# Performance work log

Measured on AMD Instinct MI355X. Metric: run time of the kernel, lower is better.

## Reference

```python
import jax, jax.numpy as jnp
import numpy as np

B, M, V, TOPK = 64, 8192, 128, 64
EPS = 1e-8  # stands in for LOG_EPS and F.cosine_similarity eps clamp


def setup_inputs() -> dict:
    key = jax.random.key(0)
    k1, k2 = jax.random.split(key)
    stdev = 1.0 / np.sqrt(M + V)
    memory = jax.random.uniform(k1, (B, M, V), dtype=jnp.float32, minval=-stdev, maxval=stdev)
    v = jax.random.normal(k2, (B, V), dtype=jnp.float32)
    return {"memory": memory, "v": v, "topk": TOPK}


def reference(memory, v, topk):
    # --- similarity(v, topk): cosine similarity of query against each memory slot ---
    a = memory + EPS                      # (B, M, V)
    b = v + EPS                           # (B, V)
    num = jnp.einsum('bmv,bv->bm', a, b)  # (B, M)
    denom = jnp.maximum(
        jnp.linalg.norm(a, axis=-1) * jnp.linalg.norm(b, axis=-1)[:, None], EPS
    )
    sim = num / denom                     # (B, M), unnormalized addressing weights
    # topk masking: torch zeroes the (M - topk) smallest entries via scatter_;
    # equivalently keep values >= the topk-th largest value (ties negligible for floats)
    kth = jax.lax.top_k(sim, topk)[0][:, -1:]   # (B, 1)
    w = jnp.where(sim >= kth, sim, jnp.zeros((), sim.dtype))
    # --- write(w, v): rank-1 outer-product update ---
    new_mem = memory + w[:, :, None] * v[:, None, :]   # (B, M, V)
    # --- read(w): weighted sum over slots; torch returns (B,1,1,V) via double unsqueeze ---
    read = jnp.einsum('bm,bmv->bv', w, new_mem)[:, None, None, :]
    return read
```

## Files before the change

kernel.cpp:

```cpp
#include <hip/hip_runtime.h>
#include <hip/hip_bf16.h>

#define B_DIM 64
#define M_DIM 8192
#define V_DIM 128
#define EPS 1e-8f
#define KCAP 2048

__device__ __forceinline__ unsigned int f2key(float f) {
    unsigned int u = __float_as_uint(f);
    return (u & 0x80000000u) ? ~u : (u | 0x80000000u);
}
__device__ __forceinline__ float key2f(unsigned int k) {
    return (k & 0x80000000u) ? __uint_as_float(k & 0x7FFFFFFFu)
                             : __uint_as_float(~k);
}

__global__ void sim_kernel(const float* __restrict__ mem,
                           const float* __restrict__ v,
                           unsigned int* __restrict__ keys_out) {
    const int b    = blockIdx.y;
    const int m0   = blockIdx.x * 64;
    const int tid  = threadIdx.x;
    const int wave = tid >> 6;
    const int lane = tid & 63;
    const int rw   = lane >> 4;
    const int sub  = lane & 15;

    __shared__ float vs[V_DIM];
    __shared__ float s_invbn;

    if (tid < V_DIM) vs[tid] = v[b * V_DIM + tid] + EPS;
    __syncthreads();

    if (tid < 64) {
        float x0 = vs[tid], x1 = vs[tid + 64];
        float s = x0 * x0 + x1 * x1;
#pragma unroll
        for (int mk = 32; mk; mk >>= 1) s += __shfl_xor(s, mk, 64);
        if (tid == 0) s_invbn = 1.0f / sqrtf(s);
    }
    __syncthreads();

    const float4 va = *reinterpret_cast<const float4*>(&vs[sub * 4]);
    const float4 vb = *reinterpret_cast<const float4*>(&vs[sub * 4 + 64]);
    const float invbn = s_invbn;

#pragma unroll
    for (int t = 0; t < 4; ++t) {
        const int m = m0 + t * 16 + wave * 4 + rw;
        const float4* rp =
            reinterpret_cast<const float4*>(mem + ((size_t)b * M_DIM + m) * V_DIM);
        float4 x0 = rp[sub];
        float4 x1 = rp[sub + 16];
        float a0 = x0.x + EPS, a1 = x0.y + EPS, a2 = x0.z + EPS, a3 = x0.w + EPS;
        float a4 = x1.x + EPS, a5 = x1.y + EPS, a6 = x1.z + EPS, a7 = x1.w + EPS;
        float dot = a0 * va.x + a1 * va.y + a2 * va.z + a3 * va.w
                  + a4 * vb.x + a5 * vb.y + a6 * vb.z + a7 * vb.w;
        float ss  = a0 * a0 + a1 * a1 + a2 * a2 + a3 * a3
                  + a4 * a4 + a5 * a5 + a6 * a6 + a7 * a7;
#pragma unroll
        for (int mk = 8; mk; mk >>= 1) {
            dot += __shfl_xor(dot, mk, 16);
            ss  += __shfl_xor(ss,  mk, 16);
        }
        if (sub == 0) {
            float sim = dot * rsqrtf(ss) * invbn;
            keys_out[(size_t)b * M_DIM + m] = f2key(sim);
        }
    }
}

__global__ void topk_read_kernel(const float* __restrict__ mem,
                                 const float* __restrict__ v,
                                 const unsigned int* __restrict__ keys_in,
                                 const int* __restrict__ topk_p,
                                 float* __restrict__ out) {
    const int b   = blockIdx.x;
    const int tid = threadIdx.x;
    const int NT  = 256;
    const int wv  = tid >> 6;

    __shared__ unsigned int keys[M_DIM];
    __shared__ unsigned int hist[4 * 256];
    __shared__ int          sfx[256];
    __shared__ unsigned int s_prefix;
    __shared__ int s_k;
    __shared__ int s_cnt;
    __shared__ int   s_idx[KCAP];
    __shared__ float s_w[KCAP];
    __shared__ float s_sumw2;
    __shared__ float s_acc[256];

    for (int i = tid; i < M_DIM; i += NT)
        keys[i] = keys_in[(size_t)b * M_DIM + i];
    if (tid == 0) { s_prefix = 0u; s_k = topk_p[0]; s_cnt = 0; }
    __syncthreads();

    for (int p = 3; p >= 0; --p) {
#pragma unroll
        for (int h = tid; h < 1024; h += NT) hist[h] = 0u;
        __syncthreads();
        const unsigned int dm = (p == 3) ? 0u : (0xFFFFFFFFu << ((p + 1) * 8));
        const unsigned int pf = s_prefix;
        const int k_cur = s_k;
        for (int i = tid; i < M_DIM; i += NT) {
            unsigned int ky = keys[i];
            if ((ky & dm) == pf)
                atomicAdd(&hist[wv * 256 + ((ky >> (p * 8)) & 0xFFu)], 1u);
        }
        __syncthreads();
        int c = (int)(hist[tid] + hist[256 + tid] + hist[512 + tid] + hist[768 + tid]);
        sfx[tid] = c;
        __syncthreads();
#pragma unroll
        for (int off = 1; off < 256; off <<= 1) {
            int x = (tid + off < 256) ? sfx[tid + off] : 0;
            __syncthreads();
            sfx[tid] += x;
            __syncthreads();
        }
        int S_t  = sfx[tid];
        int S_t1 = (tid < 255) ? sfx[tid + 1] : 0;
        if (S_t >= k_cur && S_t1 < k_cur) {
            s_prefix = pf | ((unsigned int)tid << (p * 8));
            s_k = k_cur - S_t1;
        }
        __syncthreads();
    }
    const unsigned int kth = s_prefix;

    for (int i = tid; i < M_DIM; i += NT) {
        unsigned int ky = keys[i];
        if (ky >= kth) {
            int pos = atomicAdd(&s_cnt, 1);
            if (pos < KCAP) { s_idx[pos] = i; s_w[pos] = key2f(ky); }
        }
    }
    __syncthreads();
    const int cnt = min(s_cnt, KCAP);

    if (tid < 64) {
        float s = 0.f;
        for (int i = tid; i < cnt; i += 64) s += s_w[i] * s_w[i];
#pragma unroll
        for (int mk = 32; mk; mk >>= 1) s += __shfl_xor(s, mk, 64);
        if (tid == 0) s_sumw2 = s;
    }
    __syncthreads();

    const int col  = tid & 127;
    const int half = tid >> 7;
    const float* mb = mem + (size_t)b * M_DIM * V_DIM;
    float a0 = 0.f, a1 = 0.f, a2 = 0.f, a3 = 0.f;
    int j = half;
    for (; j + 6 < cnt; j += 8) {
        a0 += s_w[j]     * mb[(size_t)s_idx[j]     * V_DIM + col];
        a1 += s_w[j + 2] * mb[(size_t)s_idx[j + 2] * V_DIM + col];
        a2 += s_w[j + 4] * mb[(size_t)s_idx[j + 4] * V_DIM + col];
        a3 += s_w[j + 6] * mb[(size_t)s_idx[j + 6] * V_DIM + col];
    }
    for (; j < cnt; j += 2)
        a0 += s_w[j] * mb[(size_t)s_idx[j] * V_DIM + col];
    s_acc[tid] = (a0 + a1) + (a2 + a3);
    __syncthreads();
    if (tid < 128)
        out[b * V_DIM + tid] =
            s_acc[tid] + s_acc[tid + 128] + s_sumw2 * v[b * V_DIM + tid];
}

extern "C" void kernel_launch(void* const* d_in, const int* in_sizes, int n_in,
                              void* d_out, int out_size, void* d_ws, size_t ws_size,
                              hipStream_t stream) {
    const float* mem  = (const float*)d_in[0];
    const float* v    = (const float*)d_in[1];
    const int*   topk = (const int*)d_in[2];
    float* out        = (float*)d_out;
    unsigned int* keys = (unsigned int*)d_ws;

    dim3 grid1(M_DIM / 64, B_DIM);
    sim_kernel<<<grid1, 256, 0, stream>>>(mem, v, keys);

    topk_read_kernel<<<B_DIM, 256, 0, stream>>>(mem, v, keys, topk, out);
}
```

Baseline: 378.7 us.

## Widen top-k block, aggregate histogram atomics, and coarsen similarity blocks

The similarity kernel now handles 256 rows per block instead of 64, and it no longer adds EPS to each memory element, which removes some arithmetic but slightly changes the numerics of the cosine. The top-k/read kernel moves from 256 to 1024 threads per block and loads keys with vector loads. Histogram updates are aggregated per wave with ballot instead of being spread over per-wave histograms, and the suffix-scan over 256 buckets is replaced by one wave using shuffles. These changes target the latency-bound selection kernel, which runs only 64 blocks, and cut barrier-heavy scans, at the cost of more complex ballot loops and a small numerical deviation.

Measured after the change: 387.3 us. 2.3% more time.

```diff
diff --git a/kernel.cpp b/kernel.cpp
--- a/kernel.cpp
+++ b/kernel.cpp
@@ -6,6 +6,7 @@
 #define V_DIM 128
 #define EPS 1e-8f
 #define KCAP 2048
+#define NT2 1024
 
 __device__ __forceinline__ unsigned int f2key(float f) {
     unsigned int u = __float_as_uint(f);
@@ -20,7 +21,7 @@
                            const float* __restrict__ v,
                            unsigned int* __restrict__ keys_out) {
     const int b    = blockIdx.y;
-    const int m0   = blockIdx.x * 64;
+    const int m0   = blockIdx.x * 256;
     const int tid  = threadIdx.x;
     const int wave = tid >> 6;
     const int lane = tid & 63;
@@ -46,19 +47,17 @@
     const float4 vb = *reinterpret_cast<const float4*>(&vs[sub * 4 + 64]);
     const float invbn = s_invbn;
 
-#pragma unroll
-    for (int t = 0; t < 4; ++t) {
+#pragma unroll 4
+    for (int t = 0; t < 16; ++t) {
         const int m = m0 + t * 16 + wave * 4 + rw;
         const float4* rp =
             reinterpret_cast<const float4*>(mem + ((size_t)b * M_DIM + m) * V_DIM);
         float4 x0 = rp[sub];
         float4 x1 = rp[sub + 16];
-        float a0 = x0.x + EPS, a1 = x0.y + EPS, a2 = x0.z + EPS, a3 = x0.w + EPS;
-        float a4 = x1.x + EPS, a5 = x1.y + EPS, a6 = x1.z + EPS, a7 = x1.w + EPS;
-        float dot = a0 * va.x + a1 * va.y + a2 * va.z + a3 * va.w
-                  + a4 * vb.x + a5 * vb.y + a6 * vb.z + a7 * vb.w;
-        float ss  = a0 * a0 + a1 * a1 + a2 * a2 + a3 * a3
-                  + a4 * a4 + a5 * a5 + a6 * a6 + a7 * a7;
+        float dot = x0.x * va.x + x0.y * va.y + x0.z * va.z + x0.w * va.w
+                  + x1.x * vb.x + x1.y * vb.y + x1.z * vb.z + x1.w * vb.w;
+        float ss  = x0.x * x0.x + x0.y * x0.y + x0.z * x0.z + x0.w * x0.w
+                  + x1.x * x1.x + x1.y * x1.y + x1.z * x1.z + x1.w * x1.w;
 #pragma unroll
         for (int mk = 8; mk; mk >>= 1) {
             dot += __shfl_xor(dot, mk, 16);
@@ -71,66 +70,88 @@
     }
 }
 
-__global__ void topk_read_kernel(const float* __restrict__ mem,
-                                 const float* __restrict__ v,
-                                 const unsigned int* __restrict__ keys_in,
-                                 const int* __restrict__ topk_p,
-                                 float* __restrict__ out) {
-    const int b   = blockIdx.x;
-    const int tid = threadIdx.x;
-    const int NT  = 256;
-    const int wv  = tid >> 6;
+__global__ __launch_bounds__(NT2)
+void topk_read_kernel(const float* __restrict__ mem,
+                      const float* __restrict__ v,
+                      const unsigned int* __restrict__ keys_in,
+                      const int* __restrict__ topk_p,
+                      float* __restrict__ out) {
+    const int b    = blockIdx.x;
+    const int tid  = threadIdx.x;
+    const int lane = tid & 63;
+    const int wv   = tid >> 6;
 
     __shared__ unsigned int keys[M_DIM];
-    __shared__ unsigned int hist[4 * 256];
-    __shared__ int          sfx[256];
+    __shared__ unsigned int hist[256];
     __shared__ unsigned int s_prefix;
     __shared__ int s_k;
     __shared__ int s_cnt;
     __shared__ int   s_idx[KCAP];
     __shared__ float s_w[KCAP];
     __shared__ float s_sumw2;
-    __shared__ float s_acc[256];
-
-    for (int i = tid; i < M_DIM; i += NT)
-        keys[i] = keys_in[(size_t)b * M_DIM + i];
+    __shared__ float s_acc[NT2];
+
+    {
+        const uint4* kin = reinterpret_cast<const uint4*>(keys_in + (size_t)b * M_DIM);
+        uint4* kl = reinterpret_cast<uint4*>(keys);
+        for (int i = tid; i < M_DIM / 4; i += NT2) kl[i] = kin[i];
+    }
     if (tid == 0) { s_prefix = 0u; s_k = topk_p[0]; s_cnt = 0; }
     __syncthreads();
 
     for (int p = 3; p >= 0; --p) {
-#pragma unroll
-        for (int h = tid; h < 1024; h += NT) hist[h] = 0u;
+        if (tid < 256) hist[tid] = 0u;
         __syncthreads();
         const unsigned int dm = (p == 3) ? 0u : (0xFFFFFFFFu << ((p + 1) * 8));
         const unsigned int pf = s_prefix;
         const int k_cur = s_k;
-        for (int i = tid; i < M_DIM; i += NT) {
+
+        for (int i = tid; i < M_DIM; i += NT2) {
             unsigned int ky = keys[i];
-            if ((ky & dm) == pf)
-                atomicAdd(&hist[wv * 256 + ((ky >> (p * 8)) & 0xFFu)], 1u);
+            bool ok = ((ky & dm) == pf);
+            int bucket = (int)((ky >> (p * 8)) & 0xFFu);
+            unsigned long long act = __ballot(ok);
+            while (act) {
+                int leader = __ffsll((long long)act) - 1;
+                int bb = __shfl(bucket, leader, 64);
+                unsigned long long match = __ballot(ok && bucket == bb);
+                if (lane == leader)
+                    atomicAdd(&hist[bb], (unsigned int)__popcll(match));
+                act &= ~match;
+            }
         }
         __syncthreads();
-        int c = (int)(hist[tid] + hist[256 + tid] + hist[512 + tid] + hist[768 + tid]);
-        sfx[tid] = c;
+
+        if (wv == 0) {
+            int c0 = (int)hist[lane * 4 + 0];
+            int c1 = (int)hist[lane * 4 + 1];
+            int c2 = (int)hist[lane * 4 + 2];
+            int c3 = (int)hist[lane * 4 + 3];
+            int s3 = c3, s2 = c2 + s3, s1 = c1 + s2, s0 = c0 + s1;
+            int T = s0, x = T;
+#pragma unroll
+            for (int off = 1; off < 64; off <<= 1) {
+                int y = __shfl_down(x, off, 64);
+                if (lane + off < 64) x += y;
+            }
+            int excl = x - T;
+            int S0 = s0 + excl, S1 = s1 + excl;
+            int S2 = s2 + excl, S3 = s3 + excl, S4 = excl;
+            int t = -1, krem = 0;
+            if (S0 >= k_cur && S1 < k_cur) { t = 0; krem = k_cur - S1; }
+            else if (S1 >= k_cur && S2 < k_cur) { t = 1; krem = k_cur - S2; }
+            else if (S2 >= k_cur && S3 < k_cur) { t = 2; krem = k_cur - S3; }
+            else if (S3 >= k_cur && S4 < k_cur) { t = 3; krem = k_cur - S4; }
+            if (t >= 0) {
+                s_prefix = pf | ((unsigned int)(lane * 4 + t) << (p * 8));
+                s_k = krem;
+            }
+        }
         __syncthreads();
-#pragma unroll
-        for (int off = 1; off < 256; off <<= 1) {
-            int x = (tid + off < 256) ? sfx[tid + off] : 0;
-            __syncthreads();
-            sfx[tid] += x;
-            __syncthreads();
-        }
-        int S_t  = sfx[tid];
-        int S_t1 = (tid < 255) ? sfx[tid + 1] : 0;
-        if (S_t >= k_cur && S_t1 < k_cur) {
-            s_prefix = pf | ((unsigned int)tid << (p * 8));
-            s_k = k_cur - S_t1;
-        }
-        __syncthreads();
     }
     const unsigned int kth = s_prefix;
 
-    for (int i = tid; i < M_DIM; i += NT) {
+    for (int i = tid; i < M_DIM; i += NT2) {
         unsigned int ky = keys[i];
         if (ky >= kth) {
             int pos = atomicAdd(&s_cnt, 1);
@@ -149,24 +170,20 @@
     }
     __syncthreads();
 
-    const int col  = tid & 127;
-    const int half = tid >> 7;
+    const int col = tid & 127;
+    const int grp = tid >> 7;
     const float* mb = mem + (size_t)b * M_DIM * V_DIM;
-    float a0 = 0.f, a1 = 0.f, a2 = 0.f, a3 = 0.f;
-    int j = half;
-    for (; j + 6 < cnt; j += 8) {
-        a0 += s_w[j]     * mb[(size_t)s_idx[j]     * V_DIM + col];
-        a1 += s_w[j + 2] * mb[(size_t)s_idx[j + 2] * V_DIM + col];
-        a2 += s_w[j + 4] * mb[(size_t)s_idx[j + 4] * V_DIM + col];
-        a3 += s_w[j + 6] * mb[(size_t)s_idx[j + 6] * V_DIM + col];
-    }
-    for (; j < cnt; j += 2)
-        a0 += s_w[j] * mb[(size_t)s_idx[j] * V_DIM + col];
-    s_acc[tid] = (a0 + a1) + (a2 + a3);
-    __syncthreads();
-    if (tid < 128)
-        out[b * V_DIM + tid] =
-            s_acc[tid] + s_acc[tid + 128] + s_sumw2 * v[b * V_DIM + tid];
+    float acc = 0.f;
+    for (int j = grp; j < cnt; j += 8)
+        acc += s_w[j] * mb[(size_t)s_idx[j] * V_DIM + col];
+    s_acc[tid] = acc;
+    __syncthreads();
+    if (tid < 128) {
+        float r = s_sumw2 * v[b * V_DIM + tid];
+#pragma unroll
+        for (int g = 0; g < 8; ++g) r += s_acc[tid + 128 * g];
+        out[b * V_DIM + tid] = r;
+    }
 }
 
 extern "C" void kernel_launch(void* const* d_in, const int* in_sizes, int n_in,
@@ -178,8 +195,8 @@
     float* out        = (float*)d_out;
     unsigned int* keys = (unsigned int*)d_ws;
 
-    dim3 grid1(M_DIM / 64, B_DIM);
+    dim3 grid1(M_DIM / 256, B_DIM);
     sim_kernel<<<grid1, 256, 0, stream>>>(mem, v, keys);
 
-    topk_read_kernel<<<B_DIM, 256, 0, stream>>>(mem, v, keys, topk, out);
-}
+    topk_read_kernel<<<B_DIM, NT2, 0, stream>>>(mem, v, keys, topk, out);
+}
```
